# Performance work log

Measured on AMD Instinct MI355X. Metric: run time of the kernel, lower is better.

The kernel has to match this reference:

```python
import jax, jax.numpy as jnp
import numpy as np

VOCAB, EMB, SEQ, UNITS, BATCH = 10000, 100, 80, 512, 2048


def setup_inputs() -> dict:
    key = jax.random.key(0)
    ks = jax.random.split(key, 8)
    s = 0.05  # param scale for numerical stability
    return {
        "ids": jax.random.randint(ks[0], (BATCH, SEQ), 0, VOCAB, dtype=jnp.int32),
        "emb": jax.random.normal(ks[1], (VOCAB, EMB), jnp.float32) * s,
        "W1": jax.random.normal(ks[2], (EMB, 4 * UNITS), jnp.float32) * s,
        "U1": jax.random.normal(ks[3], (UNITS, 4 * UNITS), jnp.float32) * s,
        "b1": jnp.zeros((4 * UNITS,), jnp.float32),
        "W2": jax.random.normal(ks[4], (UNITS, 4 * UNITS), jnp.float32) * s,
        "U2": jax.random.normal(ks[5], (UNITS, 4 * UNITS), jnp.float32) * s,
        "b2": jnp.zeros((4 * UNITS,), jnp.float32),
        "Wd": jax.random.normal(ks[6], (UNITS, 1), jnp.float32) * s,
        "bd": jnp.zeros((1,), jnp.float32),
    }


def _lstm(x, W, U, b):
    # x: [B,T,D]; Keras gate order i,f,g,o; returns (all h [B,T,U], last h [B,U])
    B = x.shape[0]
    H = U.shape[0]
    h0 = jnp.zeros((B, H), x.dtype)

    def step(carry, xt):
        h, c = carry
        z = xt @ W + h @ U + b  # [B,4H]
        i, f, g, o = jnp.split(z, 4, axis=-1)
        c = jax.nn.sigmoid(f) * c + jax.nn.sigmoid(i) * jnp.tanh(g)
        h = jax.nn.sigmoid(o) * jnp.tanh(c)
        return (h, c), h

    (hT, _), hs = jax.lax.scan(step, (h0, h0), jnp.swapaxes(x, 0, 1))
    return jnp.swapaxes(hs, 0, 1), hT


def reference(ids, emb, W1, U1, b1, W2, U2, b2, Wd, bd):
    x = emb[ids]                       # [B,T,EMB]
    x, _ = _lstm(x, W1, U1, b1)        # return_sequences=True -> [B,T,U]
    _, h = _lstm(x, W2, U2, b2)        # last hidden state [B,U]
    logits = h @ Wd + bd               # Dense(1) head
    return jax.nn.sigmoid(logits)      # [B,1]
```

## Files before the change

kernel.cpp:

```cpp
#include <hip/hip_runtime.h>
#include <hip/hip_bf16.h>

#define BATCH 2048
#define SEQ   80
#define EMBD  100
#define HU    512
#define NG    2048

typedef short bf16x8 __attribute__((ext_vector_type(8)));
typedef float f32x4  __attribute__((ext_vector_type(4)));
typedef int   i32x2  __attribute__((ext_vector_type(2)));

#define AS1(p) ((const __attribute__((address_space(1))) void*)(p))
#define AS3(p) ((__attribute__((address_space(3))) void*)(p))
#define GLL(src, dst, aux) __builtin_amdgcn_global_load_lds(AS1(src), AS3(dst), 16, 0, aux)

__global__ __launch_bounds__(256) void prep_emb(const float* __restrict__ emb,
                                                __hip_bfloat16* __restrict__ embp)
{
    int idx = blockIdx.x*256 + threadIdx.x;
    int row = idx >> 7, k = idx & 127;
    embp[idx] = __float2bfloat16(k < EMBD ? emb[row*EMBD + k] : 0.f);
}

__global__ __launch_bounds__(256) void prep_wt(
    const float* __restrict__ W1, const float* __restrict__ U1, const float* __restrict__ b1,
    const float* __restrict__ W2, const float* __restrict__ U2, const float* __restrict__ b2,
    __hip_bfloat16* __restrict__ wt1, __hip_bfloat16* __restrict__ wt2,
    float* __restrict__ bp1, float* __restrict__ bp2)
{
    const int n = blockIdx.x;
    const int u = n >> 2, g = n & 3, col = g*HU + u;
    if (blockIdx.y == 0) {
        for (int k = threadIdx.x; k < 640; k += 256) {
            float v = (k < EMBD) ? W1[k*NG + col] : ((k < 128) ? 0.f : U1[(k-128)*NG + col]);
            wt1[n*640 + k] = __float2bfloat16(v);
        }
        if (threadIdx.x == 0) bp1[n] = b1[col];
    } else {
        for (int k = threadIdx.x; k < 1024; k += 256) {
            float v = (k < HU) ? W2[k*NG + col] : U2[(k-HU)*NG + col];
            wt2[n*1024 + k] = __float2bfloat16(v);
        }
        if (threadIdx.x == 0) bp2[n] = b2[col];
    }
}

__global__ __launch_bounds__(1024, 4) void lstm_persist(
    const int* __restrict__ ids,
    const __hip_bfloat16* __restrict__ embp,
    const __hip_bfloat16* __restrict__ wt1, const float* __restrict__ bp1,
    const __hip_bfloat16* __restrict__ wt2, const float* __restrict__ bp2,
    __hip_bfloat16* __restrict__ h1a, __hip_bfloat16* __restrict__ h1b,
    __hip_bfloat16* __restrict__ h2a, __hip_bfloat16* __restrict__ h2b,
    unsigned long long* __restrict__ xbars,
    unsigned* __restrict__ slotctr)
{
    __shared__ __align__(16) char ring[4][32768];
    __shared__ int s_info;
    float* rp = (float*)&ring[0][0];

    const int tid = threadIdx.x;
    if (tid == 0) {
        unsigned x = __builtin_amdgcn_s_getreg(63508) & 7u;
        unsigned s = atomicAdd(&slotctr[x], 1u);
        s_info = (int)((x << 8) | (s & 31u));
    }
    __syncthreads();
    const int xcd  = (s_info >> 8) & 7;
    const int slot = s_info & 31;
    const int mb = slot >> 4, nb = slot & 15;
    const int m0g = xcd*256 + mb*128;
    const int n0  = nb*128;

    const int w = tid >> 6, lane = tid & 63;
    const int l15 = lane & 15, tq = lane >> 4;
    const int wM = w >> 2, wN = w & 3;
    const int khw = w >> 3;
    const int rowA = (w & 7)*16 + l15;
    const int growA = m0g + rowA;
    const int colB = n0 + rowA;
    const int erow = tid >> 3;
    const int eu8  = tid & 7;

    unsigned long long* xb = &xbars[xcd*8];

    f32x4 acc[2][2];
    float c1r[4] = {0.f,0.f,0.f,0.f};
    float c2r[4] = {0.f,0.f,0.f,0.f};

    auto zacc = [&](){
        #pragma unroll
        for (int mi = 0; mi < 2; ++mi)
            #pragma unroll
            for (int ni = 0; ni < 2; ++ni) acc[mi][ni] = (f32x4){0.f,0.f,0.f,0.f};
    };

    auto compute = [&](int buf){
        const char* base = &ring[buf][0];
        __builtin_amdgcn_s_setprio(1);
        #pragma unroll
        for (int s = 0; s < 2; ++s) {
            bf16x8 aF[2], bF[2];
            #pragma unroll
            for (int mi = 0; mi < 2; ++mi)
                aF[mi] = *(const bf16x8*)(base + (s*8 + wM*2 + mi)*1024 + tq*256 + l15*16);
            #pragma unroll
            for (int ni = 0; ni < 2; ++ni)
                bF[ni] = *(const bf16x8*)(base + 16384 + (s*8 + wN*2 + ni)*1024 + tq*256 + l15*16);
            #pragma unroll
            for (int mi = 0; mi < 2; ++mi)
                #pragma unroll
                for (int ni = 0; ni < 2; ++ni)
                    acc[mi][ni] = __builtin_amdgcn_mfma_f32_16x16x32_bf16(
                                      aF[mi], bF[ni], acc[mi][ni], 0, 0, 0);
        }
        __builtin_amdgcn_s_setprio(0);
    };

    auto epilogue = [&](const float* bp, float* cr, __hip_bfloat16* hdst){
        __syncthreads();
        #pragma unroll
        for (int mi = 0; mi < 2; ++mi)
            #pragma unroll
            for (int ni = 0; ni < 2; ++ni)
                #pragma unroll
                for (int rr = 0; rr < 4; ++rr)
                    rp[(wM*32 + mi*16 + tq*4 + rr)*132 + wN*32 + ni*16 + l15] = acc[mi][ni][rr];
        __syncthreads();
        unsigned hw[4];
        #pragma unroll
        for (int j = 0; j < 4; ++j) {
            const int ul = eu8*4 + j;
            f32x4 z  = *(const f32x4*)&rp[erow*132 + ul*4];
            f32x4 bb = *(const f32x4*)(bp + n0 + ul*4);
            const float gi = 1.f/(1.f + __expf(-(z[0] + bb[0])));
            const float gf = 1.f/(1.f + __expf(-(z[1] + bb[1])));
            const float gg = fmaf(2.f, 1.f/(1.f + __expf(-2.f*(z[2] + bb[2]))), -1.f);
            const float go = 1.f/(1.f + __expf(-(z[3] + bb[3])));
            const float cn = fmaf(gf, cr[j], gi*gg);
            cr[j] = cn;
            const float tc = fmaf(2.f, 1.f/(1.f + __expf(-2.f*cn)), -1.f);
            const float hv = go*tc;
            __hip_bfloat16 hb = __float2bfloat16(hv);
            hw[j] = (unsigned)*(const unsigned short*)&hb;
        }
        i32x2 v;
        v[0] = (int)(hw[0] | (hw[1] << 16));
        v[1] = (int)(hw[2] | (hw[3] << 16));
        *(i32x2*)(hdst + (size_t)(m0g + erow)*HU + (n0 >> 2) + eu8*4) = v;
        __syncthreads();
    };

    auto bar = [&](){
        asm volatile("s_waitcnt vmcnt(0)" ::: "memory");
        __syncthreads();
        if (tid == 0) {
            unsigned long long old = __hip_atomic_fetch_add(xb, 1ull,
                                        __ATOMIC_RELAXED, __HIP_MEMORY_SCOPE_AGENT);
            unsigned g = (unsigned)(old >> 32);
            if ((unsigned)(old & 0xffffffffull) == 31u)
                __hip_atomic_fetch_add(xb, (1ull << 32) - 32ull,
                                       __ATOMIC_RELAXED, __HIP_MEMORY_SCOPE_AGENT);
            else
                while ((unsigned)(__hip_atomic_load(xb, __ATOMIC_RELAXED,
                                        __HIP_MEMORY_SCOPE_AGENT) >> 32) == g)
                    __builtin_amdgcn_s_sleep(2);
        }
        __syncthreads();
        asm volatile("" ::: "memory");
    };

    for (int r = 0; r <= SEQ; ++r) {
        const __hip_bfloat16* h1p = ((r-1)&1) ? h1b : h1a;
        __hip_bfloat16*       h1c = (r&1)     ? h1b : h1a;
        const __hip_bfloat16* h2c = (r&1)     ? h2b : h2a;
        __hip_bfloat16*       h2p = ((r-1)&1) ? h2b : h2a;
        const __hip_bfloat16* ha1 = h1p + (size_t)growA*HU + tq*8;
        const __hip_bfloat16* ha2 = h2c + (size_t)growA*HU + tq*8;

        if (r < SEQ) {
            const int myid = ids[growA*SEQ + r];
            const __hip_bfloat16* eb = embp + (size_t)myid*128 + tq*8;
            const __hip_bfloat16* wb = wt1 + (size_t)colB*640 + tq*8;
            zacc();

            auto stage1 = [&](int kt, int buf){
                const int k0 = kt*64 + khw*32;
                if (k0 < 128) GLL(eb + k0,          &ring[buf][w*1024], 0);
                else          GLL(ha1 + (k0 - 128), &ring[buf][w*1024], 1);
                GLL(wb + k0, &ring[buf][16384 + w*1024], 0);
            };

            stage1(0, 0); stage1(1, 1); stage1(2, 2);
            #pragma unroll
            for (int i = 0; i < 10; ++i) {
                if (i < 8)       asm volatile("s_waitcnt vmcnt(4)" ::: "memory");
                else if (i == 8) asm volatile("s_waitcnt vmcnt(2)" ::: "memory");
                else             asm volatile("s_waitcnt vmcnt(0)" ::: "memory");
                __builtin_amdgcn_s_barrier();
                __builtin_amdgcn_sched_barrier(0);
                if (i + 3 < 10) stage1(i + 3, (i + 3) & 3);
                compute(i & 3);
            }
            epilogue(bp1, c1r, h1c);
        }

        if (r >= 1) {
            const __hip_bfloat16* wb = wt2 + (size_t)colB*1024 + tq*8;
            zacc();

            auto stage2 = [&](int kt, int buf){
                const int k0 = kt*64 + khw*32;
                if (k0 < 512) GLL(ha1 + k0,         &ring[buf][w*1024], 1);
                else          GLL(ha2 + (k0 - 512), &ring[buf][w*1024], 1);
                GLL(wb + k0, &ring[buf][16384 + w*1024], 0);
            };

            stage2(0, 0); stage2(1, 1); stage2(2, 2);
            #pragma unroll
            for (int i = 0; i < 16; ++i) {
                if (i < 14)       asm volatile("s_waitcnt vmcnt(4)" ::: "memory");
                else if (i == 14) asm volatile("s_waitcnt vmcnt(2)" ::: "memory");
                else              asm volatile("s_waitcnt vmcnt(0)" ::: "memory");
                __builtin_amdgcn_s_barrier();
                __builtin_amdgcn_sched_barrier(0);
                if (i + 3 < 16) stage2(i + 3, (i + 3) & 3);
                compute(i & 3);
            }
            epilogue(bp2, c2r, h2p);
        }
        bar();
    }
}

__global__ __launch_bounds__(256) void head_k(const __hip_bfloat16* __restrict__ h2,
    const float* __restrict__ Wd, const float* __restrict__ bd, float* __restrict__ out)
{
    const int b = blockIdx.x*4 + (threadIdx.x >> 6);
    const int lane = threadIdx.x & 63;
    float s = 0.f;
    #pragma unroll
    for (int u = lane; u < HU; u += 64) s += __bfloat162float(h2[b*HU + u]) * Wd[u];
    #pragma unroll
    for (int off = 32; off > 0; off >>= 1) s += __shfl_xor(s, off);
    if (lane == 0) out[b] = 1.f/(1.f + __expf(-(s + bd[0])));
}

extern "C" void kernel_launch(void* const* d_in, const int* in_sizes, int n_in,
                              void* d_out, int out_size, void* d_ws, size_t ws_size,
                              hipStream_t stream)
{
    const int*   ids = (const int*)  d_in[0];
    const float* emb = (const float*)d_in[1];
    const float* W1  = (const float*)d_in[2];
    const float* U1  = (const float*)d_in[3];
    const float* b1  = (const float*)d_in[4];
    const float* W2  = (const float*)d_in[5];
    const float* U2  = (const float*)d_in[6];
    const float* b2  = (const float*)d_in[7];
    const float* Wd  = (const float*)d_in[8];
    const float* bd  = (const float*)d_in[9];
    float* out = (float*)d_out;

    const size_t HS = (size_t)BATCH*HU;
    char* p = (char*)d_ws;
    unsigned long long* xbars = (unsigned long long*)p;
    unsigned*           slotc = (unsigned*)(p + 512);
    p += 1024;
    __hip_bfloat16* h1a = (__hip_bfloat16*)p;  p += HS*2;
    __hip_bfloat16* h1b = (__hip_bfloat16*)p;  p += HS*2;
    __hip_bfloat16* h2a = (__hip_bfloat16*)p;  p += HS*2;
    __hip_bfloat16* h2b = (__hip_bfloat16*)p;  p += HS*2;
    __hip_bfloat16* embp = (__hip_bfloat16*)p; p += (size_t)10000*128*2;
    __hip_bfloat16* wt1  = (__hip_bfloat16*)p; p += (size_t)2048*640*2;
    __hip_bfloat16* wt2  = (__hip_bfloat16*)p; p += (size_t)2048*1024*2;
    float* bp1 = (float*)p;                    p += 2048*4;
    float* bp2 = (float*)p;                    p += 2048*4;

    hipMemsetAsync(d_ws, 0, 1024 + 4*HS*2, stream);

    prep_emb<<<10000*128/256, 256, 0, stream>>>(emb, embp);
    prep_wt<<<dim3(2048,2), 256, 0, stream>>>(W1,U1,b1,W2,U2,b2, wt1,wt2,bp1,bp2);

    lstm_persist<<<256, 1024, 0, stream>>>(ids, embp, wt1, bp1, wt2, bp2,
                                           h1a, h1b, h2a, h2b, xbars, slotc);

    head_k<<<BATCH/4, 256, 0, stream>>>(h2b, Wd, bd, out);
}
```

Measured before the change: 2.855 ms.

## Fuse layer-1 and layer-2 GEMMs into one pipeline sharing h1 A-tiles

Merges the two per-step GEMM loops (layer 1 over emb+h1, layer 2 over h1+h2) into a single 18-phase pipeline. Each h1 tile loaded into LDS now feeds both layers, so the duplicate h1 loads and the second pipeline fill/drain go away. The ring is reorganised into 3 A buffers and 6 B buffers, with a prefetch depth of 2, and uses 144KB of LDS. The first and last steps now do redundant work with the writes masked off, and the higher LDS use and extra accumulator registers may reduce overlap.

```diff
diff --git a/kernel.cpp b/kernel.cpp
--- a/kernel.cpp
+++ b/kernel.cpp
@@ -14,6 +14,10 @@
 #define AS1(p) ((const __attribute__((address_space(1))) void*)(p))
 #define AS3(p) ((__attribute__((address_space(3))) void*)(p))
 #define GLL(src, dst, aux) __builtin_amdgcn_global_load_lds(AS1(src), AS3(dst), 16, 0, aux)
+
+__host__ __device__ constexpr int BIdx(int p) {
+    return (p <= 1) ? p : ((p <= 9) ? 2 + 2*(p - 2) : 18 + (p - 10));
+}
 
 __global__ __launch_bounds__(256) void prep_emb(const float* __restrict__ emb,
                                                 __hip_bfloat16* __restrict__ embp)
@@ -56,9 +60,9 @@
     unsigned long long* __restrict__ xbars,
     unsigned* __restrict__ slotctr)
 {
-    __shared__ __align__(16) char ring[4][32768];
+    __shared__ __align__(16) char smem[147456];
     __shared__ int s_info;
-    float* rp = (float*)&ring[0][0];
+    float* rp = (float*)(smem + 49152);
 
     const int tid = threadIdx.x;
     if (tid == 0) {
@@ -76,49 +80,28 @@
     const int w = tid >> 6, lane = tid & 63;
     const int l15 = lane & 15, tq = lane >> 4;
     const int wM = w >> 2, wN = w & 3;
-    const int khw = w >> 3;
     const int rowA = (w & 7)*16 + l15;
+    const int kL   = (w >> 3)*32 + tq*8;
     const int growA = m0g + rowA;
-    const int colB = n0 + rowA;
+    const int colB  = n0 + rowA;
     const int erow = tid >> 3;
     const int eu8  = tid & 7;
 
     unsigned long long* xb = &xbars[xcd*8];
 
-    f32x4 acc[2][2];
+    f32x4 acc1[2][2], acc2[2][2];
     float c1r[4] = {0.f,0.f,0.f,0.f};
     float c2r[4] = {0.f,0.f,0.f,0.f};
 
-    auto zacc = [&](){
-        #pragma unroll
-        for (int mi = 0; mi < 2; ++mi)
-            #pragma unroll
-            for (int ni = 0; ni < 2; ++ni) acc[mi][ni] = (f32x4){0.f,0.f,0.f,0.f};
+    auto Ab = [&](int p) -> char* { return smem + (((unsigned)p) % 3u)*16384; };
+    auto Bq = [&](int bi) -> char* { return smem + 49152 + (((unsigned)bi) % 6u)*16384; };
+
+    auto frag = [&](const char* base, int s, int g) -> bf16x8 {
+        return *(const bf16x8*)(base + (s*8 + g)*1024 + tq*256 + l15*16);
     };
 
-    auto compute = [&](int buf){
-        const char* base = &ring[buf][0];
-        __builtin_amdgcn_s_setprio(1);
-        #pragma unroll
-        for (int s = 0; s < 2; ++s) {
-            bf16x8 aF[2], bF[2];
-            #pragma unroll
-            for (int mi = 0; mi < 2; ++mi)
-                aF[mi] = *(const bf16x8*)(base + (s*8 + wM*2 + mi)*1024 + tq*256 + l15*16);
-            #pragma unroll
-            for (int ni = 0; ni < 2; ++ni)
-                bF[ni] = *(const bf16x8*)(base + 16384 + (s*8 + wN*2 + ni)*1024 + tq*256 + l15*16);
-            #pragma unroll
-            for (int mi = 0; mi < 2; ++mi)
-                #pragma unroll
-                for (int ni = 0; ni < 2; ++ni)
-                    acc[mi][ni] = __builtin_amdgcn_mfma_f32_16x16x32_bf16(
-                                      aF[mi], bF[ni], acc[mi][ni], 0, 0, 0);
-        }
-        __builtin_amdgcn_s_setprio(0);
-    };
-
-    auto epilogue = [&](const float* bp, float* cr, __hip_bfloat16* hdst){
+    auto epilogue = [&](f32x4 (&acc)[2][2], const float* bp, float* cr,
+                        __hip_bfloat16* hdst, bool wr){
         __syncthreads();
         #pragma unroll
         for (int mi = 0; mi < 2; ++mi)
@@ -139,16 +122,18 @@
             const float gg = fmaf(2.f, 1.f/(1.f + __expf(-2.f*(z[2] + bb[2]))), -1.f);
             const float go = 1.f/(1.f + __expf(-(z[3] + bb[3])));
             const float cn = fmaf(gf, cr[j], gi*gg);
-            cr[j] = cn;
+            if (wr) cr[j] = cn;
             const float tc = fmaf(2.f, 1.f/(1.f + __expf(-2.f*cn)), -1.f);
             const float hv = go*tc;
             __hip_bfloat16 hb = __float2bfloat16(hv);
             hw[j] = (unsigned)*(const unsigned short*)&hb;
         }
-        i32x2 v;
-        v[0] = (int)(hw[0] | (hw[1] << 16));
-        v[1] = (int)(hw[2] | (hw[3] << 16));
-        *(i32x2*)(hdst + (size_t)(m0g + erow)*HU + (n0 >> 2) + eu8*4) = v;
+        if (wr) {
+            i32x2 v;
+            v[0] = (int)(hw[0] | (hw[1] << 16));
+            v[1] = (int)(hw[2] | (hw[3] << 16));
+            *(i32x2*)(hdst + (size_t)(m0g + erow)*HU + (n0 >> 2) + eu8*4) = v;
+        }
         __syncthreads();
     };
 
@@ -176,60 +161,89 @@
         __hip_bfloat16*       h1c = (r&1)     ? h1b : h1a;
         const __hip_bfloat16* h2c = (r&1)     ? h2b : h2a;
         __hip_bfloat16*       h2p = ((r-1)&1) ? h2b : h2a;
-        const __hip_bfloat16* ha1 = h1p + (size_t)growA*HU + tq*8;
-        const __hip_bfloat16* ha2 = h2c + (size_t)growA*HU + tq*8;
-
-        if (r < SEQ) {
-            const int myid = ids[growA*SEQ + r];
-            const __hip_bfloat16* eb = embp + (size_t)myid*128 + tq*8;
-            const __hip_bfloat16* wb = wt1 + (size_t)colB*640 + tq*8;
-            zacc();
-
-            auto stage1 = [&](int kt, int buf){
-                const int k0 = kt*64 + khw*32;
-                if (k0 < 128) GLL(eb + k0,          &ring[buf][w*1024], 0);
-                else          GLL(ha1 + (k0 - 128), &ring[buf][w*1024], 1);
-                GLL(wb + k0, &ring[buf][16384 + w*1024], 0);
-            };
-
-            stage1(0, 0); stage1(1, 1); stage1(2, 2);
+
+        const int rid = (r < SEQ) ? r : (SEQ - 1);
+        const int myid = ids[growA*SEQ + rid];
+        const __hip_bfloat16* eb  = embp + (size_t)myid*128 + kL;
+        const __hip_bfloat16* ha1 = h1p + (size_t)growA*HU + kL;
+        const __hip_bfloat16* ha2 = h2c + (size_t)growA*HU + kL;
+        const __hip_bfloat16* wb1 = wt1 + (size_t)colB*640 + kL;
+        const __hip_bfloat16* wb2 = wt2 + (size_t)colB*1024 + kL;
+
+        auto stage = [&](int p){
+            char* Ad = Ab(p) + w*1024;
+            if (p < 2) {
+                GLL(eb + p*64, Ad, 0);
+                GLL(wb1 + p*64, Bq(BIdx(p)) + w*1024, 0);
+            } else if (p < 10) {
+                GLL(ha1 + (p-2)*64, Ad, 1);
+                GLL(wb1 + p*64,       Bq(BIdx(p))     + w*1024, 0);
+                GLL(wb2 + (p-2)*64,   Bq(BIdx(p) + 1) + w*1024, 0);
+            } else {
+                GLL(ha2 + (p-10)*64, Ad, 1);
+                GLL(wb2 + 512 + (p-10)*64, Bq(BIdx(p)) + w*1024, 0);
+            }
+        };
+
+        auto compute = [&](int p){
+            const char* A = Ab(p);
+            __builtin_amdgcn_s_setprio(1);
             #pragma unroll
-            for (int i = 0; i < 10; ++i) {
-                if (i < 8)       asm volatile("s_waitcnt vmcnt(4)" ::: "memory");
-                else if (i == 8) asm volatile("s_waitcnt vmcnt(2)" ::: "memory");
-                else             asm volatile("s_waitcnt vmcnt(0)" ::: "memory");
-                __builtin_amdgcn_s_barrier();
-                __builtin_amdgcn_sched_barrier(0);
-                if (i + 3 < 10) stage1(i + 3, (i + 3) & 3);
-                compute(i & 3);
+            for (int s = 0; s < 2; ++s) {
+                bf16x8 aF[2];
+                #pragma unroll
+                for (int mi = 0; mi < 2; ++mi) aF[mi] = frag(A, s, wM*2 + mi);
+                if (p < 10) {
+                    const char* B1 = Bq(BIdx(p));
+                    bf16x8 bF[2];
+                    #pragma unroll
+                    for (int ni = 0; ni < 2; ++ni) bF[ni] = frag(B1, s, wN*2 + ni);
+                    #pragma unroll
+                    for (int mi = 0; mi < 2; ++mi)
+                        #pragma unroll
+                        for (int ni = 0; ni < 2; ++ni)
+                            acc1[mi][ni] = __builtin_amdgcn_mfma_f32_16x16x32_bf16(
+                                               aF[mi], bF[ni], acc1[mi][ni], 0, 0, 0);
+                }
+                if (p >= 2) {
+                    const char* B2 = (p < 10) ? Bq(BIdx(p) + 1) : Bq(BIdx(p));
+                    bf16x8 bF[2];
+                    #pragma unroll
+                    for (int ni = 0; ni < 2; ++ni) bF[ni] = frag(B2, s, wN*2 + ni);
+                    #pragma unroll
+                    for (int mi = 0; mi < 2; ++mi)
+                        #pragma unroll
+                        for (int ni = 0; ni < 2; ++ni)
+                            acc2[mi][ni] = __builtin_amdgcn_mfma_f32_16x16x32_bf16(
+                                               aF[mi], bF[ni], acc2[mi][ni], 0, 0, 0);
+                }
             }
-            epilogue(bp1, c1r, h1c);
-        }
-
-        if (r >= 1) {
-            const __hip_bfloat16* wb = wt2 + (size_t)colB*1024 + tq*8;
-            zacc();
-
-            auto stage2 = [&](int kt, int buf){
-                const int k0 = kt*64 + khw*32;
-                if (k0 < 512) GLL(ha1 + k0,         &ring[buf][w*1024], 1);
-                else          GLL(ha2 + (k0 - 512), &ring[buf][w*1024], 1);
-                GLL(wb + k0, &ring[buf][16384 + w*1024], 0);
-            };
-
-            stage2(0, 0); stage2(1, 1); stage2(2, 2);
+            __builtin_amdgcn_s_setprio(0);
+        };
+
+        #pragma unroll
+        for (int mi = 0; mi < 2; ++mi)
             #pragma unroll
-            for (int i = 0; i < 16; ++i) {
-                if (i < 14)       asm volatile("s_waitcnt vmcnt(4)" ::: "memory");
-                else if (i == 14) asm volatile("s_waitcnt vmcnt(2)" ::: "memory");
-                else              asm volatile("s_waitcnt vmcnt(0)" ::: "memory");
-                __builtin_amdgcn_s_barrier();
-                __builtin_amdgcn_sched_barrier(0);
-                if (i + 3 < 16) stage2(i + 3, (i + 3) & 3);
-                compute(i & 3);
+            for (int ni = 0; ni < 2; ++ni) {
+                acc1[mi][ni] = (f32x4){0.f,0.f,0.f,0.f};
+                acc2[mi][ni] = (f32x4){0.f,0.f,0.f,0.f};
             }
-            epilogue(bp2, c2r, h2p);
-        }
+
+        stage(0); stage(1);
+        #pragma unroll
+        for (int p = 0; p < 18; ++p) {
+            if (p == 0)       asm volatile("s_waitcnt vmcnt(2)" ::: "memory");
+            else if (p <= 8)  asm volatile("s_waitcnt vmcnt(3)" ::: "memory");
+            else if (p <= 16) asm volatile("s_waitcnt vmcnt(2)" ::: "memory");
+            else              asm volatile("s_waitcnt vmcnt(0)" ::: "memory");
+            __builtin_amdgcn_s_barrier();
+            __builtin_amdgcn_sched_barrier(0);
+            if (p + 2 < 18) stage(p + 2);
+            compute(p);
+        }
+
+        epilogue(acc1, bp1, c1r, h1c, r < SEQ);
+        epilogue(acc2, bp2, c2r, h2p, r >= 1);
         bar();
     }
 }
```

Measured after the change: 2.731 ms. 4.4% less time.
